# Kernel tuning notes

Hardware: AMD Instinct MI355X
Metric: run time of the kernel (lower is better)

Reference implementation:

```python
import jax, jax.numpy as jnp
import numpy as np

MAX_FPS = 30.0
NUM_HEADS = 8


def _rope(x, times):
    # x: [B, H, T, D] with D even; interleaved rotary (even/odd pairs)
    B, H, T, D = x.shape
    inv_freq = 1.0 / (10000.0 ** (jnp.arange(0, D, 2, dtype=jnp.float32) / D))  # [D/2]
    pos = jnp.round(times * MAX_FPS)                       # [B, T]
    freqs = pos[:, :, None] * inv_freq[None, None, :]      # [B, T, D/2]
    cos = jnp.cos(freqs)[:, None, :, :]                    # [B, 1, T, D/2]
    sin = jnp.sin(freqs)[:, None, :, :]
    xp = x.reshape(B, H, T, D // 2, 2)
    x0, x1 = xp[..., 0], xp[..., 1]                        # even-index, odd-index elems
    r0 = x0 * cos - x1 * sin
    r1 = x0 * sin + x1 * cos
    return jnp.stack([r0, r1], axis=-1).reshape(B, H, T, D)


def setup_inputs() -> dict:
    key = jax.random.key(0)
    k1, k2, k3, k4, k5 = jax.random.split(key, 5)
    B, N, C = 4, 2048, 512
    x = jax.random.normal(k1, (B, N, C), dtype=jnp.float32)
    mask = jnp.zeros((B, N), dtype=jnp.float32)  # additive mask, 0 = attend
    # times in seconds; rounded to frame indices inside RoPE
    times = jax.random.uniform(k2, (B, N), dtype=jnp.float32) * (N / MAX_FPS)
    bound_qkv = float(np.sqrt(6.0 / (C + 3 * C)))
    Wqkv = jax.random.uniform(k3, (3 * C, C), minval=-bound_qkv, maxval=bound_qkv, dtype=jnp.float32)
    bound_p = float(np.sqrt(6.0 / (C + C)))
    Wproj = jax.random.uniform(k4, (C, C), minval=-bound_p, maxval=bound_p, dtype=jnp.float32)
    bproj = jnp.zeros((C,), dtype=jnp.float32)
    return {"x": x, "mask": mask, "times": times, "Wqkv": Wqkv,
            "Wproj": Wproj, "bproj": bproj, "num_cls_token": 0}


def reference(x, mask, times, Wqkv, Wproj, bproj, num_cls_token):
    B, N, C = x.shape
    H = NUM_HEADS
    Dh = C // H
    qkv = (x @ Wqkv.T).reshape(B, N, 3, H, Dh).transpose(2, 0, 3, 1, 4)  # [3,B,H,N,Dh]
    q, k, v = qkv[0], qkv[1], qkv[2]
    if num_cls_token > 0:
        c_q, q = q[:, :, :num_cls_token], q[:, :, num_cls_token:]
        c_k, k = k[:, :, :num_cls_token], k[:, :, num_cls_token:]
        t = times
        q = _rope(q, t)
        k = _rope(k, t)
        q = jnp.concatenate([c_q, q], axis=2)
        k = jnp.concatenate([c_k, k], axis=2)
    else:
        q = _rope(q, times)
        k = _rope(k, times)
    scale = 1.0 / jnp.sqrt(jnp.float32(Dh))
    scores = jnp.einsum('bhqd,bhkd->bhqk', q, k) * scale + mask[:, None, None, :]
    attn = jax.nn.softmax(scores, axis=-1)
    out = jnp.einsum('bhqk,bhkd->bhqd', attn, v)           # [B,H,N,Dh]
    out = out.transpose(0, 2, 1, 3).reshape(B, N, C)
    return out @ Wproj.T + bproj
```

## Files before the change

### kernel.cpp

```cpp
#include <hip/hip_runtime.h>
#include <math.h>

#define BB 4
#define NN 2048
#define CC 512
#define HH 8
#define DH 64
#define MM (BB*NN)
#define QKV_N (3*CC)
#define NSP 2
#define SLICE ((size_t)32 * NN)

typedef _Float16 f16;
typedef __attribute__((ext_vector_type(2))) _Float16 f16x2;
typedef __attribute__((ext_vector_type(4))) _Float16 f16x4;
typedef __attribute__((ext_vector_type(8))) _Float16 f16x8;
typedef __attribute__((ext_vector_type(4))) float f32x4;
typedef __attribute__((ext_vector_type(2))) __fp16 h16x2;

#define L2E 1.4426950408889634f

#define GL16(g, l) __builtin_amdgcn_global_load_lds(                       \
    (const __attribute__((address_space(1))) void*)(g),                    \
    (__attribute__((address_space(3))) void*)(l), 16, 0, 0)

#define SX4 (MM*CC/4)
#define SW4 (QKV_N*CC/4)
#define SP4 (CC*CC/4)
#define CAST_T (SX4 + SW4 + SP4)
#define TAB_T (MM * 32)
__global__ __launch_bounds__(256) void cast_tab_kernel(
    const float* __restrict__ x, const float* __restrict__ wqkv,
    const float* __restrict__ wproj, const float* __restrict__ times,
    f16* __restrict__ xh, f16* __restrict__ wqh, f16* __restrict__ wph,
    float2* __restrict__ tab)
{
    const int t = blockIdx.x * 256 + threadIdx.x;
    if (t < CAST_T) {
        const float* src; f16* dst; int i;
        if (t < SX4)            { src = x;     dst = xh;  i = t; }
        else if (t < SX4 + SW4) { src = wqkv;  dst = wqh; i = t - SX4; }
        else                    { src = wproj; dst = wph; i = t - SX4 - SW4; }
        f32x4 v = *(const f32x4*)(src + 4 * (size_t)i);
        f16x4 h = { (f16)v[0], (f16)v[1], (f16)v[2], (f16)v[3] };
        *(f16x4*)(dst + 4 * (size_t)i) = h;
    } else {
        const int idx = t - CAST_T;
        const int row = idx >> 5, fi = idx & 31;
        const float pos = rintf(times[row] * 30.0f);
        const float invf = exp2f((float)fi * (-13.287712379549449f / 32.0f));
        float s, c;
        sincosf(pos * invf, &s, &c);
        tab[idx] = make_float2(c, s);
    }
}

__global__ __launch_bounds__(256) void qkv_gemm(
    const f16* __restrict__ xh, const f16* __restrict__ wh,
    const float2* __restrict__ tab, const int* __restrict__ nclsp,
    f16* __restrict__ qo, f16* __restrict__ ksw, f16* __restrict__ vsw)
{
    __shared__ __align__(16) char smem[16896];
    f16 (*As)[32] = (f16 (*)[32])smem;
    f16 (*Bs)[32] = (f16 (*)[32])(smem + 8192);

    const int m0 = blockIdx.x * 128;
    const int n0 = blockIdx.y * 128;
    const int tid = threadIdx.x;
    const int lane = tid & 63;
    const int w = tid >> 6;
    const int wm = (w & 1) * 64, wn = (w >> 1) * 64;
    const int l15 = lane & 15, quad = lane >> 4;

    const int sr = tid >> 2;
    const int sc = (tid & 3) * 8;
    const f16* ga0 = xh + (size_t)(m0 + sr) * CC + sc;
    const f16* ga1 = xh + (size_t)(m0 + sr + 64) * CC + sc;
    const f16* gb0 = wh + (size_t)(n0 + sr) * CC + sc;
    const f16* gb1 = wh + (size_t)(n0 + sr + 64) * CC + sc;
    f16* la0 = &As[sr][sc];      f16* la1 = &As[sr + 64][sc];
    f16* lb0 = &Bs[sr][sc];      f16* lb1 = &Bs[sr + 64][sc];

    f32x4 acc[4][4] = {};
    for (int k0 = 0; k0 < CC; k0 += 32) {
        __syncthreads();
        GL16(ga0 + k0, la0);
        GL16(ga1 + k0, la1);
        GL16(gb0 + k0, lb0);
        GL16(gb1 + k0, lb1);
        __syncthreads();

        f16x8 af[4], bf[4];
        #pragma unroll
        for (int mi = 0; mi < 4; ++mi)
            af[mi] = *(const f16x8*)&As[wm + mi*16 + l15][quad * 8];
        #pragma unroll
        for (int ni = 0; ni < 4; ++ni)
            bf[ni] = *(const f16x8*)&Bs[wn + ni*16 + l15][quad * 8];
        #pragma unroll
        for (int mi = 0; mi < 4; ++mi)
            #pragma unroll
            for (int ni = 0; ni < 4; ++ni)
                acc[mi][ni] = __builtin_amdgcn_mfma_f32_16x16x32_f16(
                    af[mi], bf[ni], acc[mi][ni], 0, 0, 0);
    }
    __syncthreads();

    const int which = n0 >> 9;
    const int b     = m0 >> 11;
    const int mloc  = m0 & (NN - 1);
    const int hbase = (n0 & 511) >> 6;

    if (which < 2) {
        f16 (*Tr)[132] = (f16 (*)[132])smem;
        const int ncls = *nclsp;
        #pragma unroll
        for (int c = 0; c < 2; ++c) {
            if ((w & 1) == c) {
                #pragma unroll
                for (int mi = 0; mi < 4; ++mi)
                    #pragma unroll
                    for (int ni = 0; ni < 4; ++ni)
                        #pragma unroll
                        for (int r = 0; r < 4; ++r)
                            Tr[16*mi + quad*4 + r][wn + 16*ni + l15] =
                                (f16)acc[mi][ni][r];
            }
            __syncthreads();
            const int row = tid >> 2, cg = tid & 3;
            const int n   = mloc + c*64 + row;
            const int hh  = hbase + (cg >> 1);
            const int d0  = (cg & 1) * 32;
            f16x8 vv[4];
            #pragma unroll
            for (int j = 0; j < 4; ++j)
                vv[j] = *(const f16x8*)&Tr[row][cg*32 + j*8];
            if (n >= ncls) {
                const f32x4* t4 = (const f32x4*)(tab + ((size_t)b*NN + n)*32
                                                 + (d0 >> 1));
                #pragma unroll
                for (int j = 0; j < 4; ++j) {
                    f32x4 cs0 = t4[2*j];
                    f32x4 cs1 = t4[2*j + 1];
                    #pragma unroll
                    for (int p = 0; p < 4; ++p) {
                        const float co = (p < 2) ? cs0[(p & 1)*2]
                                                 : cs1[(p & 1)*2];
                        const float s  = (p < 2) ? cs0[(p & 1)*2 + 1]
                                                 : cs1[(p & 1)*2 + 1];
                        const float x0 = (float)vv[j][2*p];
                        const float x1 = (float)vv[j][2*p+1];
                        vv[j][2*p]   = (f16)(x0*co - x1*s);
                        vv[j][2*p+1] = (f16)(x0*s + x1*co);
                    }
                }
            }
            if (which == 0) {
                f16* qp = qo + (((size_t)(b*HH + hh))*NN + n)*DH + d0;
                #pragma unroll
                for (int j = 0; j < 4; ++j)
                    *(f16x8*)(qp + 8*j) = vv[j];
            } else {
                const int ktile = (mloc >> 6) + c;
                f16* kp = ksw + ((((size_t)(b*HH + hh))*32 + ktile)*64 + row)*64;
                #pragma unroll
                for (int j = 0; j < 4; ++j) {
                    const int blk = (d0 >> 3) + j;
                    *(f16x8*)(kp + ((blk ^ (row & 7)) * 8)) = vv[j];
                }
            }
            if (c == 0) __syncthreads();
        }
        return;
    }

    f16 (*Tv)[66] = (f16 (*)[66])smem;
    #pragma unroll
    for (int c = 0; c < 2; ++c) {
        if ((w & 1) == c) {
            #pragma unroll
            for (int mi = 0; mi < 4; ++mi)
                #pragma unroll
                for (int ni = 0; ni < 4; ++ni) {
                    f16x4 pk = { (f16)acc[mi][ni][0], (f16)acc[mi][ni][1],
                                 (f16)acc[mi][ni][2], (f16)acc[mi][ni][3] };
                    *(f16x4*)&Tv[wn + 16*ni + l15][16*mi + quad*4] = pk;
                }
        }
        __syncthreads();
        const int rr = tid >> 1;
        const int d  = rr & 63, hh = hbase + (rr >> 6);
        const int ktile = (mloc >> 6) + c;
        f16* vp = vsw + ((((size_t)(b*HH + hh))*32 + ktile)*64 + d)*64;
        #pragma unroll
        for (int j = 0; j < 4; ++j) {
            const int blk = (tid & 1)*4 + j;
            f16x8 t = *(const f16x8*)&Tv[rr][(tid & 1)*32 + j*8];
            *(f16x8*)(vp + ((blk ^ (d & 7)) * 8)) = t;
        }
        if (c == 0) __syncthreads();
    }
}

__global__ __launch_bounds__(256, 4) void attn_kernel(
    const f16* __restrict__ qg, const f16* __restrict__ ksw,
    const f16* __restrict__ vsw, const float* __restrict__ mask,
    f16* __restrict__ On, float* __restrict__ lbuf)
{
    __shared__ __align__(16) f16 asm_[4][4096];

    const int bh = blockIdx.x, qt = blockIdx.y, sp = blockIdx.z;
    const int b = bh >> 3, h = bh & 7;
    const int tid = threadIdx.x;
    const int w = tid >> 6, lane = tid & 63;
    const int l15 = lane & 15, quad = lane >> 4;
    const int rho = l15 & 7;

    const f16* qbase = qg + ((size_t)bh * NN + qt*128 + w*32) * DH;
    const f16* kt0 = ksw + ((size_t)bh * 32 + sp*16) * 4096;
    const f16* vt0 = vsw + ((size_t)bh * 32 + sp*16) * 4096;
    const float* mbase = mask + (size_t)b * NN + sp*1024;

    f16x8 Bq[2][2];
    #pragma unroll
    for (int ni = 0; ni < 2; ++ni)
        #pragma unroll
        for (int kc = 0; kc < 2; ++kc)
            Bq[ni][kc] = *(const f16x8*)(qbase + (size_t)(16*ni + l15) * DH
                                         + kc*32 + quad*8);

    const f16x4 Aones = (l15 == 0) ? f16x4{1.0f16, 1.0f16, 1.0f16, 1.0f16}
                                   : f16x4{0.0f16, 0.0f16, 0.0f16, 0.0f16};

    f32x4 O[2][4] = {};
    f32x4 Lacc[2] = {};
    const float scl = 0.125f * L2E;

    {
        const f16* ks = kt0 + tid*8;
        const f16* vs = vt0 + tid*8;
        GL16(ks,        &asm_[0][tid*8]);
        GL16(ks + 2048, &asm_[0][2048 + tid*8]);
        GL16(vs,        &asm_[1][tid*8]);
        GL16(vs + 2048, &asm_[1][2048 + tid*8]);
    }

    for (int kt = 0; kt < 16; ++kt) {
        const int cur = (kt & 1) * 2;
        __syncthreads();
        if (kt + 1 < 16) {
            const int nxt = 2 - cur;
            const f16* ks = kt0 + (size_t)(kt+1)*4096 + tid*8;
            const f16* vs = vt0 + (size_t)(kt+1)*4096 + tid*8;
            GL16(ks,        &asm_[nxt][tid*8]);
            GL16(ks + 2048, &asm_[nxt][2048 + tid*8]);
            GL16(vs,        &asm_[nxt+1][tid*8]);
            GL16(vs + 2048, &asm_[nxt+1][2048 + tid*8]);
        }
        const f16 (*Kh)[64] = (const f16 (*)[64])asm_[cur];
        const f16 (*Vt)[64] = (const f16 (*)[64])asm_[cur + 1];

        f32x4 mskv[4];
        #pragma unroll
        for (int mi = 0; mi < 4; ++mi) {
            f32x4 mv = *(const f32x4*)(mbase + kt*64 + 16*mi + quad*4);
            mskv[mi] = mv * L2E;
        }

        f32x4 st[4][2] = {};
        const int aw = (quad ^ rho) * 8;
        #pragma unroll
        for (int mi = 0; mi < 4; ++mi) {
            f16x8 Ak0 = *(const f16x8*)&Kh[16*mi + l15][aw];
            f16x8 Ak1 = *(const f16x8*)&Kh[16*mi + l15][aw ^ 32];
            #pragma unroll
            for (int ni = 0; ni < 2; ++ni) {
                st[mi][ni] = __builtin_amdgcn_mfma_f32_16x16x32_f16(Ak0, Bq[ni][0], st[mi][ni], 0, 0, 0);
                st[mi][ni] = __builtin_amdgcn_mfma_f32_16x16x32_f16(Ak1, Bq[ni][1], st[mi][ni], 0, 0, 0);
            }
        }

        f16x4 ph[4][2];
        #pragma unroll
        for (int ni = 0; ni < 2; ++ni)
            #pragma unroll
            for (int mi = 0; mi < 4; ++mi) {
                float e0 = exp2f(st[mi][ni][0] * scl + mskv[mi][0]);
                float e1 = exp2f(st[mi][ni][1] * scl + mskv[mi][1]);
                float e2 = exp2f(st[mi][ni][2] * scl + mskv[mi][2]);
                float e3 = exp2f(st[mi][ni][3] * scl + mskv[mi][3]);
                h16x2 lo = __builtin_amdgcn_cvt_pkrtz(e0, e1);
                h16x2 hi = __builtin_amdgcn_cvt_pkrtz(e2, e3);
                f16x2 lo2 = __builtin_bit_cast(f16x2, lo);
                f16x2 hi2 = __builtin_bit_cast(f16x2, hi);
                ph[mi][ni] = __builtin_shufflevector(lo2, hi2, 0, 1, 2, 3);
            }

        #pragma unroll
        for (int mi = 0; mi < 4; ++mi) {
            Lacc[0] = __builtin_amdgcn_mfma_f32_16x16x16f16(Aones, ph[mi][0], Lacc[0], 0, 0, 0);
            Lacc[1] = __builtin_amdgcn_mfma_f32_16x16x16f16(Aones, ph[mi][1], Lacc[1], 0, 0, 0);
            #pragma unroll
            for (int nd = 0; nd < 4; ++nd) {
                const int vb = ((2*mi + (quad >> 1)) ^ rho) * 8 + (quad & 1) * 4;
                f16x4 Av = *(const f16x4*)&Vt[16*nd + l15][vb];
                O[0][nd] = __builtin_amdgcn_mfma_f32_16x16x16f16(Av, ph[mi][0], O[0][nd], 0, 0, 0);
                O[1][nd] = __builtin_amdgcn_mfma_f32_16x16x16f16(Av, ph[mi][1], O[1][nd], 0, 0, 0);
            }
        }
    }

    #pragma unroll
    for (int ni = 0; ni < 2; ++ni) {
        const float l = __shfl(Lacc[ni][0], l15);
        const float inv = 1.0f / l;
        const int qrow = qt*128 + w*32 + 16*ni + l15;
        const size_t rbase = (size_t)sp * SLICE + (size_t)bh * NN + qrow;
        f16* obase = On + rbase * DH;
        #pragma unroll
        for (int nd = 0; nd < 4; ++nd) {
            f32x4 o = O[ni][nd] * inv;
            f16x4 oh = { (f16)o[0], (f16)o[1], (f16)o[2], (f16)o[3] };
            *(f16x4*)(obase + 16*nd + quad*4) = oh;
        }
        if (quad == 0)
            lbuf[rbase] = l;
    }
}

__global__ __launch_bounds__(256) void proj_gemm(
    const f16* __restrict__ On, const float* __restrict__ lbuf,
    const f16* __restrict__ wh, const float* __restrict__ bias,
    float* __restrict__ out)
{
    __shared__ f16 As[128][32];
    __shared__ f16 Bs[64][32];
    const int m0 = blockIdx.x * 128;
    const int n0 = blockIdx.y * 64;
    const int tid = threadIdx.x;
    const int lane = tid & 63;
    const int w = tid >> 6;
    const int wm = (w & 1) * 64, wn = (w >> 1) * 32;
    const int l15 = lane & 15, quad = lane >> 4;

    const int b  = m0 >> 11;
    const int q0 = m0 & (NN - 1);

    const int sr = tid >> 2;
    const int sc = (tid & 3) * 8;
    const f16* gb0 = wh + (size_t)(n0 + sr) * CC + sc;
    f16* lb0 = &Bs[sr][sc];

    f32x4 acc[4][2] = {};
    for (int k0 = 0; k0 < CC; k0 += 32) {
        const int h  = k0 >> 6;
        const int d0 = k0 & 63;
        __syncthreads();
        GL16(gb0 + k0, lb0);
        const size_t row0 = (size_t)(b*HH + h) * NN + q0 + sr;
        #pragma unroll
        for (int rr = 0; rr < 2; ++rr) {
            const size_t row = row0 + rr*64;
            const float l0 = lbuf[row], l1 = lbuf[SLICE + row];
            const float inv = 1.0f / (l0 + l1);
            const float w0 = l0 * inv, w1 = l1 * inv;
            f16x8 a0 = *(const f16x8*)(On + row * DH + d0 + sc);
            f16x8 a1 = *(const f16x8*)(On + (SLICE + row) * DH + d0 + sc);
            f16x8 o;
            #pragma unroll
            for (int r = 0; r < 8; ++r)
                o[r] = (f16)(w0 * (float)a0[r] + w1 * (float)a1[r]);
            *(f16x8*)&As[sr + rr*64][sc] = o;
        }
        __syncthreads();

        f16x8 af[4], bf[2];
        #pragma unroll
        for (int mi = 0; mi < 4; ++mi)
            af[mi] = *(const f16x8*)&As[wm + mi*16 + l15][quad * 8];
        #pragma unroll
        for (int ni = 0; ni < 2; ++ni)
            bf[ni] = *(const f16x8*)&Bs[wn + ni*16 + l15][quad * 8];
        #pragma unroll
        for (int mi = 0; mi < 4; ++mi)
            #pragma unroll
            for (int ni = 0; ni < 2; ++ni)
                acc[mi][ni] = __builtin_amdgcn_mfma_f32_16x16x32_f16(
                    af[mi], bf[ni], acc[mi][ni], 0, 0, 0);
    }

    float bb[2];
    #pragma unroll
    for (int ni = 0; ni < 2; ++ni)
        bb[ni] = bias[n0 + wn + ni*16 + l15];

    #pragma unroll
    for (int mi = 0; mi < 4; ++mi)
        #pragma unroll
        for (int r = 0; r < 4; ++r) {
            const int m = m0 + wm + mi*16 + quad*4 + r;
            #pragma unroll
            for (int ni = 0; ni < 2; ++ni)
                out[(size_t)m * CC + n0 + wn + ni*16 + l15] = acc[mi][ni][r] + bb[ni];
        }
}

extern "C" void kernel_launch(void* const* d_in, const int* in_sizes, int n_in,
                              void* d_out, int out_size, void* d_ws, size_t ws_size,
                              hipStream_t stream)
{
    const float* x     = (const float*)d_in[0];
    const float* mask  = (const float*)d_in[1];
    const float* times = (const float*)d_in[2];
    const float* Wqkv  = (const float*)d_in[3];
    const float* Wproj = (const float*)d_in[4];
    const float* bproj = (const float*)d_in[5];
    const int*   ncls  = (const int*)d_in[6];
    float* out = (float*)d_out;

    const size_t per = (size_t)BB * HH * NN * DH;
    f16* xh  = (f16*)d_ws;
    f16* wqh = xh + per;
    f16* wph = wqh + (size_t)QKV_N * CC;
    f16* q   = wph + (size_t)CC * CC;
    f16* ks  = q + per;
    f16* vs  = ks + per;
    f16* On  = vs + per;
    float* lb = (float*)(On + NSP * per);
    float2* tab = (float2*)(lb + NSP * 32 * NN);

    cast_tab_kernel<<<(CAST_T + TAB_T) / 256, 256, 0, stream>>>(
        x, Wqkv, Wproj, times, xh, wqh, wph, tab);
    qkv_gemm<<<dim3(MM / 128, QKV_N / 128), 256, 0, stream>>>(
        xh, wqh, tab, ncls, q, ks, vs);
    attn_kernel<<<dim3(BB * HH, NN / 128, NSP), 256, 0, stream>>>(
        q, ks, vs, mask, On, lb);
    proj_gemm<<<dim3(MM / 128, CC / 64), 256, 0, stream>>>(
        On, lb, wph, bproj, out);
}
```

Measured before the change: 191.5 us.

## Fold softmax scale into Wq and additive mask into V weights

Pre-scales the Q rows of Wqkv by 0.125*log2(e) during the cast, so attention scores come out already in the exp2 domain. The additive mask is turned into multiplicative f16 weights exp2(mask*L2E), which are folded into V in the QKV epilogue and into the row-sum MFMA's A operand. This drops the per-score FMA and mask loads from the attention inner loop and uses the hardware exp2 instruction. In exchange it adds a small table pass, and since there is no running max it depends on scores staying bounded. Masks of -inf or very large magnitude could underflow the f16 weights.

```diff
diff --git a/kernel.cpp b/kernel.cpp
--- a/kernel.cpp
+++ b/kernel.cpp
@@ -19,6 +19,17 @@
 typedef __attribute__((ext_vector_type(2))) __fp16 h16x2;
 
 #define L2E 1.4426950408889634f
+#define QSCL (0.125f * L2E)
+
+__device__ __forceinline__ float fast_exp2(float x) {
+#if __has_builtin(__builtin_amdgcn_exp2f)
+    return __builtin_amdgcn_exp2f(x);
+#else
+    float r;
+    asm volatile("v_exp_f32 %0, %1\n\ts_nop 1" : "=v"(r) : "v"(x));
+    return r;
+#endif
+}
 
 #define GL16(g, l) __builtin_amdgcn_global_load_lds(                       \
     (const __attribute__((address_space(1))) void*)(g),                    \
@@ -29,22 +40,27 @@
 #define SP4 (CC*CC/4)
 #define CAST_T (SX4 + SW4 + SP4)
 #define TAB_T (MM * 32)
+#define WT_T  (MM / 8)
 __global__ __launch_bounds__(256) void cast_tab_kernel(
     const float* __restrict__ x, const float* __restrict__ wqkv,
     const float* __restrict__ wproj, const float* __restrict__ times,
+    const float* __restrict__ mask,
     f16* __restrict__ xh, f16* __restrict__ wqh, f16* __restrict__ wph,
-    float2* __restrict__ tab)
+    float2* __restrict__ tab, f16* __restrict__ wtab)
 {
     const int t = blockIdx.x * 256 + threadIdx.x;
     if (t < CAST_T) {
         const float* src; f16* dst; int i;
+        bool qscale = false;
         if (t < SX4)            { src = x;     dst = xh;  i = t; }
-        else if (t < SX4 + SW4) { src = wqkv;  dst = wqh; i = t - SX4; }
+        else if (t < SX4 + SW4) { src = wqkv;  dst = wqh; i = t - SX4;
+                                  qscale = (i < CC*CC/4); }
         else                    { src = wproj; dst = wph; i = t - SX4 - SW4; }
         f32x4 v = *(const f32x4*)(src + 4 * (size_t)i);
+        if (qscale) v *= QSCL;
         f16x4 h = { (f16)v[0], (f16)v[1], (f16)v[2], (f16)v[3] };
         *(f16x4*)(dst + 4 * (size_t)i) = h;
-    } else {
+    } else if (t < CAST_T + TAB_T) {
         const int idx = t - CAST_T;
         const int row = idx >> 5, fi = idx & 31;
         const float pos = rintf(times[row] * 30.0f);
@@ -52,12 +68,24 @@
         float s, c;
         sincosf(pos * invf, &s, &c);
         tab[idx] = make_float2(c, s);
+    } else {
+        const int i = t - CAST_T - TAB_T;
+        f32x4 m0 = *(const f32x4*)(mask + 8 * (size_t)i);
+        f32x4 m1 = *(const f32x4*)(mask + 8 * (size_t)i + 4);
+        f16x8 wv;
+        #pragma unroll
+        for (int r = 0; r < 4; ++r) {
+            wv[r]     = (f16)fast_exp2(m0[r] * L2E);
+            wv[4 + r] = (f16)fast_exp2(m1[r] * L2E);
+        }
+        *(f16x8*)(wtab + 8 * (size_t)i) = wv;
     }
 }
 
 __global__ __launch_bounds__(256) void qkv_gemm(
     const f16* __restrict__ xh, const f16* __restrict__ wh,
     const float2* __restrict__ tab, const int* __restrict__ nclsp,
+    const f16* __restrict__ wtab,
     f16* __restrict__ qo, f16* __restrict__ ksw, f16* __restrict__ vsw)
 {
     __shared__ __align__(16) char smem[16896];
@@ -196,6 +224,8 @@
         for (int j = 0; j < 4; ++j) {
             const int blk = (tid & 1)*4 + j;
             f16x8 t = *(const f16x8*)&Tv[rr][(tid & 1)*32 + j*8];
+            t *= *(const f16x8*)&wtab[(size_t)b*NN + mloc + c*64
+                                      + (tid & 1)*32 + j*8];
             *(f16x8*)(vp + ((blk ^ (d & 7)) * 8)) = t;
         }
         if (c == 0) __syncthreads();
@@ -204,13 +234,13 @@
 
 __global__ __launch_bounds__(256, 4) void attn_kernel(
     const f16* __restrict__ qg, const f16* __restrict__ ksw,
-    const f16* __restrict__ vsw, const float* __restrict__ mask,
+    const f16* __restrict__ vsw, const f16* __restrict__ wtab,
     f16* __restrict__ On, float* __restrict__ lbuf)
 {
     __shared__ __align__(16) f16 asm_[4][4096];
 
     const int bh = blockIdx.x, qt = blockIdx.y, sp = blockIdx.z;
-    const int b = bh >> 3, h = bh & 7;
+    const int b = bh >> 3;
     const int tid = threadIdx.x;
     const int w = tid >> 6, lane = tid & 63;
     const int l15 = lane & 15, quad = lane >> 4;
@@ -219,7 +249,7 @@
     const f16* qbase = qg + ((size_t)bh * NN + qt*128 + w*32) * DH;
     const f16* kt0 = ksw + ((size_t)bh * 32 + sp*16) * 4096;
     const f16* vt0 = vsw + ((size_t)bh * 32 + sp*16) * 4096;
-    const float* mbase = mask + (size_t)b * NN + sp*1024;
+    const f16* wsl = wtab + (size_t)b * NN + sp*1024;
 
     f16x8 Bq[2][2];
     #pragma unroll
@@ -229,12 +259,10 @@
             Bq[ni][kc] = *(const f16x8*)(qbase + (size_t)(16*ni + l15) * DH
                                          + kc*32 + quad*8);
 
-    const f16x4 Aones = (l15 == 0) ? f16x4{1.0f16, 1.0f16, 1.0f16, 1.0f16}
-                                   : f16x4{0.0f16, 0.0f16, 0.0f16, 0.0f16};
-
+    const f16x4 zf4 = {};
+    const f32x4 fz = {};
     f32x4 O[2][4] = {};
     f32x4 Lacc[2] = {};
-    const float scl = 0.125f * L2E;
 
     {
         const f16* ks = kt0 + tid*8;
@@ -260,14 +288,14 @@
         const f16 (*Kh)[64] = (const f16 (*)[64])asm_[cur];
         const f16 (*Vt)[64] = (const f16 (*)[64])asm_[cur + 1];
 
-        f32x4 mskv[4];
+        f16x4 Aw[4];
         #pragma unroll
         for (int mi = 0; mi < 4; ++mi) {
-            f32x4 mv = *(const f32x4*)(mbase + kt*64 + 16*mi + quad*4);
-            mskv[mi] = mv * L2E;
-        }
-
-        f32x4 st[4][2] = {};
+            f16x4 wv = *(const f16x4*)(wsl + kt*64 + 16*mi + quad*4);
+            Aw[mi] = (l15 == 0) ? wv : zf4;
+        }
+
+        f32x4 st[4][2];
         const int aw = (quad ^ rho) * 8;
         #pragma unroll
         for (int mi = 0; mi < 4; ++mi) {
@@ -275,8 +303,10 @@
             f16x8 Ak1 = *(const f16x8*)&Kh[16*mi + l15][aw ^ 32];
             #pragma unroll
             for (int ni = 0; ni < 2; ++ni) {
-                st[mi][ni] = __builtin_amdgcn_mfma_f32_16x16x32_f16(Ak0, Bq[ni][0], st[mi][ni], 0, 0, 0);
-                st[mi][ni] = __builtin_amdgcn_mfma_f32_16x16x32_f16(Ak1, Bq[ni][1], st[mi][ni], 0, 0, 0);
+                f32x4 t0 = __builtin_amdgcn_mfma_f32_16x16x32_f16(
+                    Ak0, Bq[ni][0], fz, 0, 0, 0);
+                st[mi][ni] = __builtin_amdgcn_mfma_f32_16x16x32_f16(
+                    Ak1, Bq[ni][1], t0, 0, 0, 0);
             }
         }
 
@@ -285,10 +315,10 @@
         for (int ni = 0; ni < 2; ++ni)
             #pragma unroll
             for (int mi = 0; mi < 4; ++mi) {
-                float e0 = exp2f(st[mi][ni][0] * scl + mskv[mi][0]);
-                float e1 = exp2f(st[mi][ni][1] * scl + mskv[mi][1]);
-                float e2 = exp2f(st[mi][ni][2] * scl + mskv[mi][2]);
-                float e3 = exp2f(st[mi][ni][3] * scl + mskv[mi][3]);
+                float e0 = fast_exp2(st[mi][ni][0]);
+                float e1 = fast_exp2(st[mi][ni][1]);
+                float e2 = fast_exp2(st[mi][ni][2]);
+                float e3 = fast_exp2(st[mi][ni][3]);
                 h16x2 lo = __builtin_amdgcn_cvt_pkrtz(e0, e1);
                 h16x2 hi = __builtin_amdgcn_cvt_pkrtz(e2, e3);
                 f16x2 lo2 = __builtin_bit_cast(f16x2, lo);
@@ -298,8 +328,8 @@
 
         #pragma unroll
         for (int mi = 0; mi < 4; ++mi) {
-            Lacc[0] = __builtin_amdgcn_mfma_f32_16x16x16f16(Aones, ph[mi][0], Lacc[0], 0, 0, 0);
-            Lacc[1] = __builtin_amdgcn_mfma_f32_16x16x16f16(Aones, ph[mi][1], Lacc[1], 0, 0, 0);
+            Lacc[0] = __builtin_amdgcn_mfma_f32_16x16x16f16(Aw[mi], ph[mi][0], Lacc[0], 0, 0, 0);
+            Lacc[1] = __builtin_amdgcn_mfma_f32_16x16x16f16(Aw[mi], ph[mi][1], Lacc[1], 0, 0, 0);
             #pragma unroll
             for (int nd = 0; nd < 4; ++nd) {
                 const int vb = ((2*mi + (quad >> 1)) ^ rho) * 8 + (quad & 1) * 4;
@@ -428,13 +458,14 @@
     f16* On  = vs + per;
     float* lb = (float*)(On + NSP * per);
     float2* tab = (float2*)(lb + NSP * 32 * NN);
-
-    cast_tab_kernel<<<(CAST_T + TAB_T) / 256, 256, 0, stream>>>(
-        x, Wqkv, Wproj, times, xh, wqh, wph, tab);
+    f16* wtab = (f16*)(tab + (size_t)MM * 32);
+
+    cast_tab_kernel<<<(CAST_T + TAB_T + WT_T) / 256, 256, 0, stream>>>(
+        x, Wqkv, Wproj, times, mask, xh, wqh, wph, tab, wtab);
     qkv_gemm<<<dim3(MM / 128, QKV_N / 128), 256, 0, stream>>>(
-        xh, wqh, tab, ncls, q, ks, vs);
+        xh, wqh, tab, ncls, wtab, q, ks, vs);
     attn_kernel<<<dim3(BB * HH, NN / 128, NSP), 256, 0, stream>>>(
-        q, ks, vs, mask, On, lb);
+        q, ks, vs, wtab, On, lb);
     proj_gemm<<<dim3(MM / 128, CC / 64), 256, 0, stream>>>(
         On, lb, wph, bproj, out);
 }
```

Measured after the change: 174.8 us. 1.1x faster.
